# Performance work log

Hardware: AMD Instinct MI355X
Metric: run time of the kernel (lower is better)

The kernel has to match this reference:

```python
import jax, jax.numpy as jnp
import numpy as np

B, S, D, H = 2, 2048, 1024, 16
HD = D // H


def setup_inputs() -> dict:
    key = jax.random.key(0)
    ks = jax.random.split(key, 9)
    sc = 0.02
    return {
        "x": jax.random.normal(ks[0], (B, S, D), dtype=jnp.float32),
        "qw": jax.random.normal(ks[1], (D, D), dtype=jnp.float32) * sc,
        "qb": jax.random.normal(ks[2], (D,), dtype=jnp.float32) * sc,
        "kw": jax.random.normal(ks[3], (D, D), dtype=jnp.float32) * sc,
        "kb": jax.random.normal(ks[4], (D,), dtype=jnp.float32) * sc,
        "vw": jax.random.normal(ks[5], (D, D), dtype=jnp.float32) * sc,
        "vb": jax.random.normal(ks[6], (D,), dtype=jnp.float32) * sc,
        "ow": jax.random.normal(ks[7], (D, D), dtype=jnp.float32) * sc,
        "ob": jax.random.normal(ks[8], (D,), dtype=jnp.float32) * sc,
    }


def reference(x, qw, qb, kw, kb, vw, vb, ow, ob):
    b, s, d = x.shape
    # projections (torch Linear: x @ W.T + b)
    q = (x @ qw.T + qb).reshape(b, s, H, HD).transpose(0, 2, 1, 3)  # bhsd
    k = (x @ kw.T + kb).reshape(b, s, H, HD).transpose(0, 2, 1, 3)
    v = (x @ vw.T + vb).reshape(b, s, H, HD).transpose(0, 2, 1, 3)
    scale = 1.0 / jnp.sqrt(jnp.float32(HD))
    score = jnp.einsum("bhsd,bhtd->bhst", q, k) * scale  # bhss
    # causal mask: -inf strictly above diagonal
    mask = jnp.triu(jnp.full((s, s), -jnp.inf, dtype=score.dtype), k=1)
    score = jax.nn.softmax(score + mask, axis=-1)
    o = jnp.einsum("bhst,bhtd->bhsd", score, v)
    o = o.transpose(0, 2, 1, 3).reshape(b, s, d)
    return o @ ow.T + ob
```

## Files before the change

kernel.cpp:

```cpp
#include <hip/hip_runtime.h>
#include <hip/hip_bf16.h>
#include <stdint.h>

typedef __bf16 bf16x8 __attribute__((ext_vector_type(8)));
typedef __bf16 bf16x4 __attribute__((ext_vector_type(4)));
typedef float f32x4 __attribute__((ext_vector_type(4)));
typedef unsigned short ushort_t;


__device__ inline ushort_t f2bf(float f) {
  union { float f; uint32_t u; } v; v.f = f;
  uint32_t r = (v.u + 0x7fffu + ((v.u >> 16) & 1u)) >> 16;
  return (ushort_t)r;
}

__device__ inline void gll16(const void* g, void* l) {
  __builtin_amdgcn_global_load_lds((const __attribute__((address_space(1))) void*)g,
                                   (__attribute__((address_space(3))) void*)l, 16, 0, 0);
}

__global__ void cvt_all(const float* __restrict__ x,
                        const float* __restrict__ qw, const float* __restrict__ kw,
                        const float* __restrict__ vw, const float* __restrict__ ow,
                        ushort_t* __restrict__ xb, ushort_t* __restrict__ wb) {
  int bid = blockIdx.x;
  const float* s;
  ushort_t* o;
  int i;
  if (bid < 4096) {
    s = x; o = xb; i = bid * 256 + threadIdx.x;
  } else {
    int j = bid - 4096;
    int wi = j >> 10;
    const float* srcs[4] = {qw, kw, vw, ow};
    s = srcs[wi];
    o = wb + (size_t)wi * 1048576;
    i = (j & 1023) * 256 + threadIdx.x;
  }
  float4 f = ((const float4*)s)[i];
  union { ushort_t u[4]; uint2 v; } r;
  r.u[0] = f2bf(f.x); r.u[1] = f2bf(f.y); r.u[2] = f2bf(f.z); r.u[3] = f2bf(f.w);
  ((uint2*)o)[i] = r.v;
}

#define NKT 16

__device__ inline void stage_half(const ushort_t* __restrict__ g, ushort_t* l, int tid) {
  #pragma unroll
  for (int i = 0; i < 2; i++) {
    int c = tid + i * 512;
    int row = c >> 3;
    int q = (c & 7) ^ (row & 7);
    gll16(g + (size_t)row * 1024 + q * 8, l + c * 8);
  }
}

__global__ __launch_bounds__(512, 2) void qkv_gemm(
    const ushort_t* __restrict__ xb,
    const ushort_t* __restrict__ qwb, const ushort_t* __restrict__ kwb, const ushort_t* __restrict__ vwb,
    const float* __restrict__ qbias, const float* __restrict__ kbias, const float* __restrict__ vbias,
    ushort_t* __restrict__ qo, ushort_t* __restrict__ ko, ushort_t* __restrict__ vto)
{
  const int z = blockIdx.y;
  const int bx = blockIdx.x;
  const float* bias = (z == 0) ? qbias : (z == 1) ? kbias : vbias;
  const ushort_t* Ap;
  const ushort_t* Bp;
  int m0, n0;
  if (z == 2) {
    Ap = vwb; Bp = xb;
    m0 = (bx & 3) * 256;
    n0 = (bx >> 2) * 256;
  } else {
    Ap = xb; Bp = (z == 0) ? qwb : kwb;
    m0 = (bx >> 2) * 256;
    n0 = (bx & 3) * 256;
  }

  __shared__ __align__(16) ushort_t As[2][2][128 * 64];
  __shared__ __align__(16) ushort_t Bs[2][2][128 * 64];

  const int tid = threadIdx.x;
  const int w = tid >> 6;
  const int lane = tid & 63;
  const int ln = lane & 15;
  const int q4 = lane >> 4;
  const int wm = w & 1;
  const int wn = w >> 1;
  const int bh = wn >> 1;
  const int brow0 = (wn & 1) * 64;

  f32x4 acc[8][4];
  #pragma unroll
  for (int i = 0; i < 8; i++)
    #pragma unroll
    for (int j = 0; j < 4; j++) acc[i][j] = f32x4{0.f, 0.f, 0.f, 0.f};

  stage_half(Ap + (size_t)(m0 +   0) * 1024 +  0, &As[0][0][0], tid);
  stage_half(Ap + (size_t)(m0 + 128) * 1024 +  0, &As[0][1][0], tid);
  stage_half(Bp + (size_t)(n0 +   0) * 1024 +  0, &Bs[0][0][0], tid);
  stage_half(Bp + (size_t)(n0 + 128) * 1024 +  0, &Bs[0][1][0], tid);
  stage_half(Bp + (size_t)(n0 +   0) * 1024 + 64, &Bs[1][0][0], tid);
  stage_half(Bp + (size_t)(n0 + 128) * 1024 + 64, &Bs[1][1][0], tid);
  asm volatile("s_waitcnt vmcnt(4)" ::: "memory");
  __builtin_amdgcn_s_barrier();

  const int achk = ln & 7;

  for (int t = 0; t < NKT; ++t) {
    const int buf = t & 1;
    const ushort_t* Abuf = &As[buf][wm][0];
    const ushort_t* Bbuf = &Bs[buf][bh][0];

    bf16x8 a0[4][2], a4[4][2], b0[2][2], b2[2][2];

    #pragma unroll
    for (int m = 0; m < 4; m++)
      #pragma unroll
      for (int ks = 0; ks < 2; ks++)
        a0[m][ks] = *(const bf16x8*)&Abuf[(m * 16 + ln) * 64 + (((ks * 4 + q4) ^ achk) * 8)];
    #pragma unroll
    for (int n = 0; n < 2; n++)
      #pragma unroll
      for (int ks = 0; ks < 2; ks++)
        b0[n][ks] = *(const bf16x8*)&Bbuf[(brow0 + n * 16 + ln) * 64 + (((ks * 4 + q4) ^ achk) * 8)];
    if (t + 1 < NKT)
      stage_half(Ap + (size_t)m0 * 1024 + (t + 1) * 64, &As[(t + 1) & 1][0][0], tid);
    __builtin_amdgcn_s_barrier();
    asm volatile("s_waitcnt lgkmcnt(0)" ::: "memory");
    __builtin_amdgcn_s_setprio(1);
    #pragma unroll
    for (int m = 0; m < 4; m++)
      #pragma unroll
      for (int n = 0; n < 2; n++)
        #pragma unroll
        for (int ks = 0; ks < 2; ks++)
          acc[m][n] = __builtin_amdgcn_mfma_f32_16x16x32_bf16(a0[m][ks], b0[n][ks], acc[m][n], 0, 0, 0);
    __builtin_amdgcn_s_setprio(0);
    __builtin_amdgcn_s_barrier();

    #pragma unroll
    for (int n = 0; n < 2; n++)
      #pragma unroll
      for (int ks = 0; ks < 2; ks++)
        b2[n][ks] = *(const bf16x8*)&Bbuf[(brow0 + (n + 2) * 16 + ln) * 64 + (((ks * 4 + q4) ^ achk) * 8)];
    if (t + 1 < NKT)
      stage_half(Ap + (size_t)(m0 + 128) * 1024 + (t + 1) * 64, &As[(t + 1) & 1][1][0], tid);
    __builtin_amdgcn_s_barrier();
    asm volatile("s_waitcnt lgkmcnt(0)" ::: "memory");
    __builtin_amdgcn_s_setprio(1);
    #pragma unroll
    for (int m = 0; m < 4; m++)
      #pragma unroll
      for (int n = 0; n < 2; n++)
        #pragma unroll
        for (int ks = 0; ks < 2; ks++)
          acc[m][n + 2] = __builtin_amdgcn_mfma_f32_16x16x32_bf16(a0[m][ks], b2[n][ks], acc[m][n + 2], 0, 0, 0);
    __builtin_amdgcn_s_setprio(0);
    __builtin_amdgcn_s_barrier();

    #pragma unroll
    for (int m = 0; m < 4; m++)
      #pragma unroll
      for (int ks = 0; ks < 2; ks++)
        a4[m][ks] = *(const bf16x8*)&Abuf[((m + 4) * 16 + ln) * 64 + (((ks * 4 + q4) ^ achk) * 8)];
    if (t + 2 < NKT)
      stage_half(Bp + (size_t)n0 * 1024 + (t + 2) * 64, &Bs[buf][0][0], tid);
    __builtin_amdgcn_s_barrier();
    asm volatile("s_waitcnt lgkmcnt(0)" ::: "memory");
    __builtin_amdgcn_s_setprio(1);
    #pragma unroll
    for (int m = 0; m < 4; m++)
      #pragma unroll
      for (int n = 0; n < 2; n++)
        #pragma unroll
        for (int ks = 0; ks < 2; ks++)
          acc[m + 4][n + 2] = __builtin_amdgcn_mfma_f32_16x16x32_bf16(a4[m][ks], b2[n][ks], acc[m + 4][n + 2], 0, 0, 0);
    __builtin_amdgcn_s_setprio(0);
    __builtin_amdgcn_s_barrier();

    if (t + 2 < NKT)
      stage_half(Bp + (size_t)(n0 + 128) * 1024 + (t + 2) * 64, &Bs[buf][1][0], tid);
    __builtin_amdgcn_s_barrier();
    __builtin_amdgcn_s_setprio(1);
    #pragma unroll
    for (int m = 0; m < 4; m++)
      #pragma unroll
      for (int n = 0; n < 2; n++)
        #pragma unroll
        for (int ks = 0; ks < 2; ks++)
          acc[m + 4][n] = __builtin_amdgcn_mfma_f32_16x16x32_bf16(a4[m][ks], b0[n][ks], acc[m + 4][n], 0, 0, 0);
    __builtin_amdgcn_s_setprio(0);
    if (t + 2 < NKT) {
      asm volatile("s_waitcnt vmcnt(4)" ::: "memory");
    } else if (t + 1 < NKT) {
      asm volatile("s_waitcnt vmcnt(0)" ::: "memory");
    }
    __builtin_amdgcn_s_barrier();
  }

  if (z == 2) {
    #pragma unroll
    for (int n = 0; n < 4; n++) {
      int col = n0 + wn * 64 + n * 16 + ln;
      int bb = col >> 11, s = col & 2047;
      size_t base = (size_t)bb * 2097152 + s;
      #pragma unroll
      for (int m = 0; m < 8; m++) {
        int prow = m0 + wm * 128 + m * 16 + q4 * 4;
        #pragma unroll
        for (int r = 0; r < 4; r++) {
          int p = prow + r;
          vto[base + (size_t)p * 2048] = f2bf(acc[m][n][r] + bias[p]);
        }
      }
    }
  } else {
    #pragma unroll
    for (int n = 0; n < 4; n++) {
      int col = n0 + wn * 64 + n * 16 + ln;
      float bv = bias[col];
      int h = col >> 6, hd = col & 63;
      #pragma unroll
      for (int m = 0; m < 8; m++) {
        int rowb = m0 + wm * 128 + m * 16 + q4 * 4;
        #pragma unroll
        for (int r = 0; r < 4; r++) {
          int row = rowb + r;
          int b = row >> 11, s = row & 2047;
          float val = acc[m][n][r] + bv;
          if (z == 0) {
            qo[((size_t)((b * 16 + h) * 2048 + s)) * 64 + hd] = f2bf(val * 0.180336884f);
          } else {
            ko[((size_t)((b * 16 + h) * 2048 + s)) * 64 + hd] = f2bf(val);
          }
        }
      }
    }
  }
}

#define PPAD 68
__global__ __launch_bounds__(512) void attn(
    const ushort_t* __restrict__ qp, const ushort_t* __restrict__ kp,
    const ushort_t* __restrict__ vtp, ushort_t* __restrict__ op)
{
  __shared__ __align__(16) ushort_t Ks[2][64 * 64];
  __shared__ __align__(16) ushort_t Vts[2][64 * 64];
  __shared__ __align__(16) ushort_t Ps[8][16 * PPAD];

  const int tid = threadIdx.x;
  const int w = tid >> 6;
  const int lane = tid & 63;
  const int ln = lane & 15;
  const int q4 = lane >> 4;
  const int bh = blockIdx.y;
  const int b = bh >> 4, h = bh & 15;
  int tswz = (blockIdx.x + blockIdx.y) & 15;
  const int qt = (blockIdx.y & 16) ? (15 - tswz) : tswz;
  const int q0 = qt * 128;
  const int nt = 2 * qt + 2;

  const int sr_row = tid >> 3;
  const int sr_q = (tid & 7) ^ (sr_row & 7);

  bf16x8 onesf;
  {
    union { ushort_t u[8]; bf16x8 v; } t;
    #pragma unroll
    for (int j = 0; j < 8; j++) t.u[j] = 0x3F80;
    onesf = t.v;
  }

  bf16x8 qf[2];
  {
    const ushort_t* base = qp + ((size_t)bh * 2048 + q0 + w * 16 + ln) * 64 + q4 * 8;
    qf[0] = *(const bf16x8*)(base);
    qf[1] = *(const bf16x8*)(base + 32);
  }

  f32x4 acc_o[4];
  f32x4 acc_l = f32x4{0.f, 0.f, 0.f, 0.f};
  #pragma unroll
  for (int t = 0; t < 4; t++) acc_o[t] = f32x4{0.f, 0.f, 0.f, 0.f};

  const ushort_t* kb = kp + (size_t)bh * 2048 * 64;
  const ushort_t* vb = vtp + (size_t)bh * 64 * 2048;

  gll16(kb + (size_t)sr_row * 64 + sr_q * 8, &Ks[0][tid * 8]);
  gll16(vb + (size_t)sr_row * 2048 + sr_q * 8, &Vts[0][tid * 8]);
  asm volatile("s_waitcnt vmcnt(0)" ::: "memory");
  __builtin_amdgcn_s_barrier();

  const int fchk = ln & 7;

  for (int it = 0; it < nt; it++) {
    const int cur = it & 1;
    if (it + 1 < nt) {
      int kv1 = (it + 1) * 64;
      gll16(kb + (size_t)(kv1 + sr_row) * 64 + sr_q * 8, &Ks[cur ^ 1][tid * 8]);
      gll16(vb + (size_t)sr_row * 2048 + kv1 + sr_q * 8, &Vts[cur ^ 1][tid * 8]);
    }

    f32x4 sc[4];
    #pragma unroll
    for (int t = 0; t < 4; t++) sc[t] = f32x4{0.f, 0.f, 0.f, 0.f};
    __builtin_amdgcn_s_setprio(1);
    #pragma unroll
    for (int ks = 0; ks < 2; ks++) {
      bf16x8 kf[4];
      #pragma unroll
      for (int tn = 0; tn < 4; tn++)
        kf[tn] = *(const bf16x8*)(&Ks[cur][(tn * 16 + ln) * 64 + (((ks * 4 + q4) ^ fchk) * 8)]);
      #pragma unroll
      for (int tn = 0; tn < 4; tn++)
        sc[tn] = __builtin_amdgcn_mfma_f32_16x16x32_bf16(qf[ks], kf[tn], sc[tn], 0, 0, 0);
    }
    __builtin_amdgcn_s_setprio(0);

    if (it >= 2 * qt) {
      int qrow = q0 + w * 16 + q4 * 4;
      int kv0 = it * 64;
      #pragma unroll
      for (int tn = 0; tn < 4; tn++) {
        int col = kv0 + tn * 16 + ln;
        #pragma unroll
        for (int r = 0; r < 4; r++)
          if (col > qrow + r) sc[tn][r] = -__builtin_inff();
      }
    }
    #pragma unroll
    for (int tn = 0; tn < 4; tn++)
      #pragma unroll
      for (int r = 0; r < 4; r++) {
        float p = __builtin_amdgcn_exp2f(sc[tn][r]);
        Ps[w][(q4 * 4 + r) * PPAD + tn * 16 + ln] = (ushort_t)(__float_as_uint(p) >> 16);
      }
    __builtin_amdgcn_s_setprio(1);
    #pragma unroll
    for (int ks = 0; ks < 2; ks++) {
      bf16x8 vf[4];
      #pragma unroll
      for (int tn = 0; tn < 4; tn++)
        vf[tn] = *(const bf16x8*)(&Vts[cur][(tn * 16 + ln) * 64 + (((ks * 4 + q4) ^ fchk) * 8)]);
      const ushort_t* pp = &Ps[w][ln * PPAD + ks * 32 + q4 * 8];
      bf16x4 plo = *(const bf16x4*)(pp);
      bf16x4 phi = *(const bf16x4*)(pp + 4);
      bf16x8 pf = __builtin_shufflevector(plo, phi, 0, 1, 2, 3, 4, 5, 6, 7);
      acc_l = __builtin_amdgcn_mfma_f32_16x16x32_bf16(pf, onesf, acc_l, 0, 0, 0);
      #pragma unroll
      for (int tn = 0; tn < 4; tn++)
        acc_o[tn] = __builtin_amdgcn_mfma_f32_16x16x32_bf16(pf, vf[tn], acc_o[tn], 0, 0, 0);
    }
    __builtin_amdgcn_s_setprio(0);

    if (it + 1 < nt) {
      asm volatile("s_waitcnt vmcnt(0)" ::: "memory");
      __builtin_amdgcn_s_barrier();
    }
  }

  {
    float invl[4];
    #pragma unroll
    for (int r = 0; r < 4; r++) invl[r] = __builtin_amdgcn_rcpf(acc_l[r]);
    #pragma unroll
    for (int tn = 0; tn < 4; tn++)
      #pragma unroll
      for (int r = 0; r < 4; r++) {
        int row = q0 + w * 16 + q4 * 4 + r;
        op[((size_t)b * 2048 + row) * 1024 + h * 64 + tn * 16 + ln] =
            f2bf(acc_o[tn][r] * invl[r]);
      }
  }
}

__global__ __launch_bounds__(256) void out_gemm(
    const ushort_t* __restrict__ ob_in, const ushort_t* __restrict__ owb,
    const float* __restrict__ obias, float* __restrict__ out)
{
  __shared__ __align__(16) ushort_t As[3][64 * 64];
  __shared__ __align__(16) ushort_t Bs[3][128 * 64];

  const int tid = threadIdx.x;
  const int w = tid >> 6;
  const int lane = tid & 63;
  const int ln = lane & 15;
  const int q4 = lane >> 4;
  const int wm = w & 1, wn = w >> 1;
  const int m0 = blockIdx.y * 64;
  const int n0 = blockIdx.x * 128;

  f32x4 acc[2][4];
  #pragma unroll
  for (int i = 0; i < 2; i++)
    #pragma unroll
    for (int j = 0; j < 4; j++) acc[i][j] = f32x4{0.f, 0.f, 0.f, 0.f};

  auto STAGE = [&](int bi, int k0) {
    #pragma unroll
    for (int i = 0; i < 2; i++) {
      int c = tid + i * 256;
      int row = c >> 3;
      int cq = (c & 7) ^ (row & 7);
      gll16(&ob_in[(size_t)(m0 + row) * 1024 + k0 + cq * 8], &As[bi][c * 8]);
    }
    #pragma unroll
    for (int i = 0; i < 4; i++) {
      int c = tid + i * 256;
      int row = c >> 3;
      int cq = (c & 7) ^ (row & 7);
      gll16(&owb[(size_t)(n0 + row) * 1024 + k0 + cq * 8], &Bs[bi][c * 8]);
    }
  };

  STAGE(0, 0);
  STAGE(1, 64);
  asm volatile("s_waitcnt vmcnt(6)" ::: "memory");
  __builtin_amdgcn_s_barrier();

  #pragma unroll
  for (int t = 0; t < 16; t++) {
    const int cb = t % 3;
    if (t + 2 < 16) STAGE((t + 2) % 3, (t + 2) * 64);
    #pragma unroll
    for (int ks = 0; ks < 2; ks++) {
      bf16x8 af[2], bfr[4];
      #pragma unroll
      for (int tt = 0; tt < 2; tt++) {
        int rr = wm * 32 + tt * 16 + ln;
        af[tt] = *(const bf16x8*)(&As[cb][rr * 64 + (((ks * 4 + q4) ^ (rr & 7)) * 8)]);
      }
      #pragma unroll
      for (int tt = 0; tt < 4; tt++) {
        int rc = wn * 64 + tt * 16 + ln;
        bfr[tt] = *(const bf16x8*)(&Bs[cb][rc * 64 + (((ks * 4 + q4) ^ (rc & 7)) * 8)]);
      }
      #pragma unroll
      for (int tm = 0; tm < 2; tm++)
        #pragma unroll
        for (int tn = 0; tn < 4; tn++)
          acc[tm][tn] = __builtin_amdgcn_mfma_f32_16x16x32_bf16(af[tm], bfr[tn], acc[tm][tn], 0, 0, 0);
    }
    if (t + 2 < 16) {
      asm volatile("s_waitcnt vmcnt(6)" ::: "memory");
    } else if (t + 1 < 16) {
      asm volatile("s_waitcnt vmcnt(0)" ::: "memory");
    }
    __builtin_amdgcn_s_barrier();
  }

  #pragma unroll
  for (int tn = 0; tn < 4; tn++) {
    int col = n0 + wn * 64 + tn * 16 + ln;
    float bv = obias[col];
    #pragma unroll
    for (int tm = 0; tm < 2; tm++) {
      int rowb = m0 + wm * 32 + tm * 16 + q4 * 4;
      #pragma unroll
      for (int r = 0; r < 4; r++)
        out[(size_t)(rowb + r) * 1024 + col] = acc[tm][tn][r] + bv;
    }
  }
}

extern "C" void kernel_launch(void* const* d_in, const int* in_sizes, int n_in,
                              void* d_out, int out_size, void* d_ws, size_t ws_size,
                              hipStream_t stream) {
  const float* x     = (const float*)d_in[0];
  const float* qw    = (const float*)d_in[1];
  const float* qb    = (const float*)d_in[2];
  const float* kw    = (const float*)d_in[3];
  const float* kb    = (const float*)d_in[4];
  const float* vw    = (const float*)d_in[5];
  const float* vb    = (const float*)d_in[6];
  const float* ow    = (const float*)d_in[7];
  const float* obias = (const float*)d_in[8];
  float* out = (float*)d_out;

  char* ws = (char*)d_ws;
  ushort_t* xb  = (ushort_t*)(ws);
  ushort_t* wb  = (ushort_t*)(ws + 8388608);
  ushort_t* qwb = wb;
  ushort_t* kwb = wb + 1048576;
  ushort_t* vwb = wb + 2097152;
  ushort_t* owb = wb + 3145728;
  ushort_t* qo  = (ushort_t*)(ws + 16777216);
  ushort_t* ko  = (ushort_t*)(ws + 25165824);
  ushort_t* vto = (ushort_t*)(ws + 33554432);
  ushort_t* oo  = (ushort_t*)(ws + 41943040);

  cvt_all<<<dim3(8192), dim3(256), 0, stream>>>(x, qw, kw, vw, ow, xb, wb);

  qkv_gemm<<<dim3(64, 3), dim3(512), 0, stream>>>(xb, qwb, kwb, vwb, qb, kb, vb, qo, ko, vto);
  attn<<<dim3(16, 32), dim3(512), 0, stream>>>(qo, ko, vto, oo);
  out_gemm<<<dim3(8, 64), dim3(256), 0, stream>>>(oo, owb, obias, out);
}
```

Baseline: 186.4 us.

## Process two 16-row query subtiles per wave in attention with 256 threads

The attention kernel now uses 4 waves per block instead of 8, and each wave handles 32 query rows as two 16-row subtiles. K and V fragments read from LDS are reused across both subtiles, which halves LDS fragment reads per MFMA. Each thread issues two async global-to-LDS loads per tile instead of one. Register pressure per wave roughly doubles for accumulators, and there are fewer waves per block to hide latency.

```diff
diff --git a/kernel.cpp b/kernel.cpp
--- a/kernel.cpp
+++ b/kernel.cpp
@@ -241,7 +241,7 @@
 }
 
 #define PPAD 68
-__global__ __launch_bounds__(512) void attn(
+__global__ __launch_bounds__(256) void attn(
     const ushort_t* __restrict__ qp, const ushort_t* __restrict__ kp,
     const ushort_t* __restrict__ vtp, ushort_t* __restrict__ op)
 {
@@ -261,8 +261,9 @@
   const int q0 = qt * 128;
   const int nt = 2 * qt + 2;
 
-  const int sr_row = tid >> 3;
-  const int sr_q = (tid & 7) ^ (sr_row & 7);
+  const int c0 = tid, c1 = tid + 256;
+  const int r0_ = c0 >> 3, q0_ = (c0 & 7) ^ (r0_ & 7);
+  const int r1_ = c1 >> 3, q1_ = (c1 & 7) ^ (r1_ & 7);
 
   bf16x8 onesf;
   {
@@ -272,23 +273,30 @@
     onesf = t.v;
   }
 
-  bf16x8 qf[2];
-  {
-    const ushort_t* base = qp + ((size_t)bh * 2048 + q0 + w * 16 + ln) * 64 + q4 * 8;
-    qf[0] = *(const bf16x8*)(base);
-    qf[1] = *(const bf16x8*)(base + 32);
-  }
-
-  f32x4 acc_o[4];
-  f32x4 acc_l = f32x4{0.f, 0.f, 0.f, 0.f};
-  #pragma unroll
-  for (int t = 0; t < 4; t++) acc_o[t] = f32x4{0.f, 0.f, 0.f, 0.f};
+  bf16x8 qf[2][2];
+  #pragma unroll
+  for (int s = 0; s < 2; s++) {
+    const ushort_t* base = qp + ((size_t)bh * 2048 + q0 + w * 32 + s * 16 + ln) * 64 + q4 * 8;
+    qf[s][0] = *(const bf16x8*)(base);
+    qf[s][1] = *(const bf16x8*)(base + 32);
+  }
+
+  f32x4 acc_o[2][4];
+  f32x4 acc_l[2];
+  #pragma unroll
+  for (int s = 0; s < 2; s++) {
+    acc_l[s] = f32x4{0.f, 0.f, 0.f, 0.f};
+    #pragma unroll
+    for (int t = 0; t < 4; t++) acc_o[s][t] = f32x4{0.f, 0.f, 0.f, 0.f};
+  }
 
   const ushort_t* kb = kp + (size_t)bh * 2048 * 64;
   const ushort_t* vb = vtp + (size_t)bh * 64 * 2048;
 
-  gll16(kb + (size_t)sr_row * 64 + sr_q * 8, &Ks[0][tid * 8]);
-  gll16(vb + (size_t)sr_row * 2048 + sr_q * 8, &Vts[0][tid * 8]);
+  gll16(kb + (size_t)r0_ * 64 + q0_ * 8, &Ks[0][c0 * 8]);
+  gll16(kb + (size_t)r1_ * 64 + q1_ * 8, &Ks[0][c1 * 8]);
+  gll16(vb + (size_t)r0_ * 2048 + q0_ * 8, &Vts[0][c0 * 8]);
+  gll16(vb + (size_t)r1_ * 2048 + q1_ * 8, &Vts[0][c1 * 8]);
   asm volatile("s_waitcnt vmcnt(0)" ::: "memory");
   __builtin_amdgcn_s_barrier();
 
@@ -298,13 +306,17 @@
     const int cur = it & 1;
     if (it + 1 < nt) {
       int kv1 = (it + 1) * 64;
-      gll16(kb + (size_t)(kv1 + sr_row) * 64 + sr_q * 8, &Ks[cur ^ 1][tid * 8]);
-      gll16(vb + (size_t)sr_row * 2048 + kv1 + sr_q * 8, &Vts[cur ^ 1][tid * 8]);
-    }
-
-    f32x4 sc[4];
-    #pragma unroll
-    for (int t = 0; t < 4; t++) sc[t] = f32x4{0.f, 0.f, 0.f, 0.f};
+      gll16(kb + (size_t)(kv1 + r0_) * 64 + q0_ * 8, &Ks[cur ^ 1][c0 * 8]);
+      gll16(kb + (size_t)(kv1 + r1_) * 64 + q1_ * 8, &Ks[cur ^ 1][c1 * 8]);
+      gll16(vb + (size_t)r0_ * 2048 + kv1 + q0_ * 8, &Vts[cur ^ 1][c0 * 8]);
+      gll16(vb + (size_t)r1_ * 2048 + kv1 + q1_ * 8, &Vts[cur ^ 1][c1 * 8]);
+    }
+
+    f32x4 sc[2][4];
+    #pragma unroll
+    for (int s = 0; s < 2; s++)
+      #pragma unroll
+      for (int t = 0; t < 4; t++) sc[s][t] = f32x4{0.f, 0.f, 0.f, 0.f};
     __builtin_amdgcn_s_setprio(1);
     #pragma unroll
     for (int ks = 0; ks < 2; ks++) {
@@ -313,29 +325,36 @@
       for (int tn = 0; tn < 4; tn++)
         kf[tn] = *(const bf16x8*)(&Ks[cur][(tn * 16 + ln) * 64 + (((ks * 4 + q4) ^ fchk) * 8)]);
       #pragma unroll
+      for (int s = 0; s < 2; s++)
+        #pragma unroll
+        for (int tn = 0; tn < 4; tn++)
+          sc[s][tn] = __builtin_amdgcn_mfma_f32_16x16x32_bf16(qf[s][ks], kf[tn], sc[s][tn], 0, 0, 0);
+    }
+    __builtin_amdgcn_s_setprio(0);
+
+    if (it >= 2 * qt) {
+      int kv0 = it * 64;
+      #pragma unroll
+      for (int s = 0; s < 2; s++) {
+        int qrow = q0 + w * 32 + s * 16 + q4 * 4;
+        #pragma unroll
+        for (int tn = 0; tn < 4; tn++) {
+          int col = kv0 + tn * 16 + ln;
+          #pragma unroll
+          for (int r = 0; r < 4; r++)
+            if (col > qrow + r) sc[s][tn][r] = -__builtin_inff();
+        }
+      }
+    }
+    #pragma unroll
+    for (int s = 0; s < 2; s++)
+      #pragma unroll
       for (int tn = 0; tn < 4; tn++)
-        sc[tn] = __builtin_amdgcn_mfma_f32_16x16x32_bf16(qf[ks], kf[tn], sc[tn], 0, 0, 0);
-    }
-    __builtin_amdgcn_s_setprio(0);
-
-    if (it >= 2 * qt) {
-      int qrow = q0 + w * 16 + q4 * 4;
-      int kv0 = it * 64;
-      #pragma unroll
-      for (int tn = 0; tn < 4; tn++) {
-        int col = kv0 + tn * 16 + ln;
-        #pragma unroll
-        for (int r = 0; r < 4; r++)
-          if (col > qrow + r) sc[tn][r] = -__builtin_inff();
-      }
-    }
-    #pragma unroll
-    for (int tn = 0; tn < 4; tn++)
-      #pragma unroll
-      for (int r = 0; r < 4; r++) {
-        float p = __builtin_amdgcn_exp2f(sc[tn][r]);
-        Ps[w][(q4 * 4 + r) * PPAD + tn * 16 + ln] = (ushort_t)(__float_as_uint(p) >> 16);
-      }
+        #pragma unroll
+        for (int r = 0; r < 4; r++) {
+          float p = __builtin_amdgcn_exp2f(sc[s][tn][r]);
+          Ps[w * 2 + s][(q4 * 4 + r) * PPAD + tn * 16 + ln] = (ushort_t)(__float_as_uint(p) >> 16);
+        }
     __builtin_amdgcn_s_setprio(1);
     #pragma unroll
     for (int ks = 0; ks < 2; ks++) {
@@ -343,14 +362,17 @@
       #pragma unroll
       for (int tn = 0; tn < 4; tn++)
         vf[tn] = *(const bf16x8*)(&Vts[cur][(tn * 16 + ln) * 64 + (((ks * 4 + q4) ^ fchk) * 8)]);
-      const ushort_t* pp = &Ps[w][ln * PPAD + ks * 32 + q4 * 8];
-      bf16x4 plo = *(const bf16x4*)(pp);
-      bf16x4 phi = *(const bf16x4*)(pp + 4);
-      bf16x8 pf = __builtin_shufflevector(plo, phi, 0, 1, 2, 3, 4, 5, 6, 7);
-      acc_l = __builtin_amdgcn_mfma_f32_16x16x32_bf16(pf, onesf, acc_l, 0, 0, 0);
-      #pragma unroll
-      for (int tn = 0; tn < 4; tn++)
-        acc_o[tn] = __builtin_amdgcn_mfma_f32_16x16x32_bf16(pf, vf[tn], acc_o[tn], 0, 0, 0);
+      #pragma unroll
+      for (int s = 0; s < 2; s++) {
+        const ushort_t* pp = &Ps[w * 2 + s][ln * PPAD + ks * 32 + q4 * 8];
+        bf16x4 plo = *(const bf16x4*)(pp);
+        bf16x4 phi = *(const bf16x4*)(pp + 4);
+        bf16x8 pf = __builtin_shufflevector(plo, phi, 0, 1, 2, 3, 4, 5, 6, 7);
+        acc_l[s] = __builtin_amdgcn_mfma_f32_16x16x32_bf16(pf, onesf, acc_l[s], 0, 0, 0);
+        #pragma unroll
+        for (int tn = 0; tn < 4; tn++)
+          acc_o[s][tn] = __builtin_amdgcn_mfma_f32_16x16x32_bf16(pf, vf[tn], acc_o[s][tn], 0, 0, 0);
+      }
     }
     __builtin_amdgcn_s_setprio(0);
 
@@ -360,17 +382,18 @@
     }
   }
 
-  {
+  #pragma unroll
+  for (int s = 0; s < 2; s++) {
     float invl[4];
     #pragma unroll
-    for (int r = 0; r < 4; r++) invl[r] = __builtin_amdgcn_rcpf(acc_l[r]);
+    for (int r = 0; r < 4; r++) invl[r] = __builtin_amdgcn_rcpf(acc_l[s][r]);
     #pragma unroll
     for (int tn = 0; tn < 4; tn++)
       #pragma unroll
       for (int r = 0; r < 4; r++) {
-        int row = q0 + w * 16 + q4 * 4 + r;
+        int row = q0 + w * 32 + s * 16 + q4 * 4 + r;
         op[((size_t)b * 2048 + row) * 1024 + h * 64 + tn * 16 + ln] =
-            f2bf(acc_o[tn][r] * invl[r]);
+            f2bf(acc_o[s][tn][r] * invl[r]);
       }
   }
 }
@@ -493,6 +516,6 @@
   cvt_all<<<dim3(8192), dim3(256), 0, stream>>>(x, qw, kw, vw, ow, xb, wb);
 
   qkv_gemm<<<dim3(64, 3), dim3(512), 0, stream>>>(xb, qwb, kwb, vwb, qb, kb, vb, qo, ko, vto);
-  attn<<<dim3(16, 32), dim3(512), 0, stream>>>(qo, ko, vto, oo);
+  attn<<<dim3(16, 32), dim3(256), 0, stream>>>(qo, ko, vto, oo);
   out_gemm<<<dim3(8, 64), dim3(256), 0, stream>>>(oo, owb, obias, out);
 }
```

New measurement: 188.9 us. No clear change (+1.4%).
